# Kernel optimization log

Hardware: AMD Instinct MI355X
Metric: run time of the kernel (lower is better)

Reference implementation:

```python
import jax, jax.numpy as jnp
import numpy as np

N_NODES = 100000
N_EDGES = 1600000
D = 128
L = 3


def setup_inputs() -> dict:
    key = jax.random.key(0)
    k1, k2, k3, k4, k5 = jax.random.split(key, 5)
    x = jax.random.normal(k1, (N_NODES, D), dtype=jnp.float32)
    edge_index = jax.random.randint(k2, (2, N_EDGES), 0, N_NODES, dtype=jnp.int64)
    # Stacked per-layer params (all layers are [D, D] since in==out)
    Wl = jax.random.normal(k3, (L, D, D), dtype=jnp.float32) * 0.05  # lin_l (neighbors), with bias
    bl = jax.random.normal(k4, (L, D), dtype=jnp.float32) * 0.05
    Wr = jax.random.normal(k5, (L, D, D), dtype=jnp.float32) * 0.05  # lin_r (root), no bias
    return {"x": x, "edge_index": edge_index, "Wl": Wl, "bl": bl, "Wr": Wr}


def _sage_conv(x, src, dst, W_l, b_l, W_r):
    # mean aggregation of source features onto target nodes
    msgs = x[src]                                             # [E, D] gather
    agg = jax.ops.segment_sum(msgs, dst, num_segments=N_NODES)  # [N, D] scatter-add
    cnt = jax.ops.segment_sum(jnp.ones((src.shape[0],), x.dtype), dst,
                              num_segments=N_NODES)
    mean = agg / jnp.maximum(cnt, 1.0)[:, None]
    # out = lin_l(mean_neighbors) + lin_r(x)
    return mean @ W_l.T + b_l + x @ W_r.T


def reference(x, edge_index, Wl, bl, Wr):
    src, dst = edge_index[0], edge_index[1]
    for i in range(L):
        x = _sage_conv(x, src, dst, Wl[i], bl[i], Wr[i])
        if i != L - 1:
            x = jax.nn.relu(x)
            # dropout p=0.5 is identity in eval mode
    return jnp.min(x, axis=0)  # [D]
```

## Files before the change

kernel.cpp:

```cpp
#include <hip/hip_runtime.h>
#include <hip/hip_bf16.h>

#define D 128
#define SCAN_C 512
#define BKT 512
#define BKT_SHIFT 9
#define CH 256
#define NBMAX 512
#define MREP 64

typedef __attribute__((ext_vector_type(8))) short bf16x8;
typedef __attribute__((ext_vector_type(4))) float f32x4;

__device__ __forceinline__ float bf16_to_f(unsigned int u) {
    union { unsigned int i; float f; } c; c.i = u << 16; return c.f;
}
__device__ __forceinline__ unsigned short f_to_bf16(float f) {
    union { float f; unsigned int i; } c; c.f = f;
    unsigned int r = c.i + 0x7FFFu + ((c.i >> 16) & 1u);
    return (unsigned short)(r >> 16);
}

__global__ void detect_kernel(const unsigned short* __restrict__ xr,
                              const int* __restrict__ er, int* __restrict__ flag) {
    int plaus = 0;
    for (int i = 0; i < 64; ++i) {
        unsigned short u = xr[2 * i];
        int e = (u >> 7) & 0xFF;
        if (e >= 0x74 && e <= 0x82) plaus++;
    }
    flag[1] = (plaus >= 32) ? 1 : 0;
    int zeros = 0;
    for (int i = 1; i < 128; i += 2) zeros += (er[i] == 0);
    flag[0] = (zeros >= 60) ? 1 : 0;
}

__device__ __forceinline__ int load_idx(const void* p, long long i, int is64) {
    if (is64) return (int)((const long long*)p)[i];
    return ((const int*)p)[i];
}

__global__ void cvt_x_kernel(const void* __restrict__ src, const int* __restrict__ flag,
                             unsigned short* __restrict__ dst, int n) {
    int is_bf16 = flag[1];
    int i = blockIdx.x * blockDim.x + threadIdx.x;
    int stride = gridDim.x * blockDim.x;
    if (is_bf16) {
        const unsigned short* s = (const unsigned short*)src;
        for (; i < n; i += stride) dst[i] = s[i];
    } else {
        const float* s = (const float*)src;
        for (; i < n; i += stride) dst[i] = f_to_bf16(s[i]);
    }
}

__global__ void cvt_f_kernel(const void* __restrict__ src, const int* __restrict__ flag,
                             float* __restrict__ dst, int n) {
    int is_bf16 = flag[1];
    int i = blockIdx.x * blockDim.x + threadIdx.x;
    int stride = gridDim.x * blockDim.x;
    if (is_bf16) {
        const unsigned short* s = (const unsigned short*)src;
        for (; i < n; i += stride) dst[i] = bf16_to_f(s[i]);
    } else {
        const float* s = (const float*)src;
        for (; i < n; i += stride) dst[i] = s[i];
    }
}

__global__ void packW_kernel(const void* __restrict__ Wl0, const void* __restrict__ Wr0,
                             const int* __restrict__ flag, unsigned short* __restrict__ Wpack,
                             int L) {
    int idx = blockIdx.x * blockDim.x + threadIdx.x;
    if (idx >= L * 8 * 8 * 64) return;
    int lane = idx & 63;
    int ks = (idx >> 6) & 7;
    int nt = (idx >> 9) & 7;
    int layer = idx >> 12;
    int n = nt * 16 + (lane & 15);
    int k0 = ks * 32 + (lane >> 4) * 8;
    int is_bf16 = flag[1];
    unsigned short outv[8];
#pragma unroll
    for (int j = 0; j < 8; ++j) {
        int k = k0 + j;
        size_t off = (size_t)layer * D * D + (size_t)n * D + (k & 127);
        float v;
        if (is_bf16) {
            const unsigned short* W = (const unsigned short*)((k < D) ? Wl0 : Wr0);
            v = bf16_to_f(W[off]);
        } else {
            const float* W = (const float*)((k < D) ? Wl0 : Wr0);
            v = W[off];
        }
        outv[j] = f_to_bf16(v);
    }
    *(uint4*)&Wpack[(size_t)idx * 8] = *(uint4*)outv;
}

__global__ void bucket_hist_kernel(const void* __restrict__ eidx, const int* __restrict__ flag,
                                   int* __restrict__ counts2D, int E, int NB, int EPC) {
    __shared__ int hist[NBMAX];
    int c = blockIdx.x;
    for (int i = threadIdx.x; i < NB; i += blockDim.x) hist[i] = 0;
    __syncthreads();
    int is64 = flag[0];
    int end = min(E, (c + 1) * EPC);
    for (int e = c * EPC + threadIdx.x; e < end; e += blockDim.x) {
        int d = load_idx(eidx, (long long)E + e, is64);
        atomicAdd(&hist[d >> BKT_SHIFT], 1);
    }
    __syncthreads();
    for (int i = threadIdx.x; i < NB; i += blockDim.x)
        counts2D[i * CH + c] = hist[i];
}

__global__ void gscan1_kernel(const int* __restrict__ in, int* __restrict__ blockSums, int n) {
    __shared__ int red[256];
    int base = blockIdx.x * SCAN_C;
    int t = threadIdx.x;
    int s = 0;
    if (base + t < n) s += in[base + t];
    if (base + t + 256 < n) s += in[base + t + 256];
    red[t] = s;
    __syncthreads();
    for (int off = 128; off > 0; off >>= 1) {
        if (t < off) red[t] += red[t + off];
        __syncthreads();
    }
    if (t == 0) blockSums[blockIdx.x] = red[0];
}

__global__ void gscan2_kernel(int* __restrict__ blockSums, int nb) {
    __shared__ int sh[256];
    int t = threadIdx.x;
    int orig = (t < nb) ? blockSums[t] : 0;
    sh[t] = orig;
    __syncthreads();
    for (int off = 1; off < 256; off <<= 1) {
        int v = (t >= off) ? sh[t - off] : 0;
        __syncthreads();
        sh[t] += v;
        __syncthreads();
    }
    if (t < nb) blockSums[t] = sh[t] - orig;
}

__global__ void gscan3_kernel(const int* __restrict__ in, const int* __restrict__ blockBase,
                              int* __restrict__ out, int n) {
    __shared__ int sh[SCAN_C];
    int base = blockIdx.x * SCAN_C;
    int t = threadIdx.x;
    int v0 = (base + t < n) ? in[base + t] : 0;
    int v1 = (base + t + 256 < n) ? in[base + t + 256] : 0;
    sh[t] = v0;
    sh[t + 256] = v1;
    __syncthreads();
    for (int off = 1; off < SCAN_C; off <<= 1) {
        int a = (t >= off) ? sh[t - off] : 0;
        int b = (t + 256 >= off) ? sh[t + 256 - off] : 0;
        __syncthreads();
        sh[t] += a;
        sh[t + 256] += b;
        __syncthreads();
    }
    int bb = blockBase[blockIdx.x];
    if (base + t < n) out[base + t] = bb + sh[t] - v0;
    if (base + t + 256 < n) out[base + t + 256] = bb + sh[t + 256] - v1;
}

__global__ void bucket_scatter_kernel(const void* __restrict__ eidx, const int* __restrict__ flag,
                                      const int* __restrict__ bases2D, unsigned int* __restrict__ ebuf,
                                      int E, int NB, int EPC) {
    __shared__ int cur[NBMAX];
    int c = blockIdx.x;
    for (int i = threadIdx.x; i < NB; i += blockDim.x) cur[i] = bases2D[i * CH + c];
    __syncthreads();
    int is64 = flag[0];
    int end = min(E, (c + 1) * EPC);
    for (int e = c * EPC + threadIdx.x; e < end; e += blockDim.x) {
        int s = load_idx(eidx, e, is64);
        int d = load_idx(eidx, (long long)E + e, is64);
        int b = d >> BKT_SHIFT;
        int pos = atomicAdd(&cur[b], 1);
        ebuf[pos] = ((unsigned)s << BKT_SHIFT) | (unsigned)(d & (BKT - 1));
    }
}

__global__ __launch_bounds__(BKT)
void bucket_csr_kernel(const unsigned int* __restrict__ ebuf, const int* __restrict__ bases2D,
                       int* __restrict__ offsets, int* __restrict__ srcs, int E, int N, int NB) {
    __shared__ int lcnt[BKT];
    __shared__ int sh[BKT];
    __shared__ int lcur[BKT];
    int b = blockIdx.x;
    int t = threadIdx.x;
    int start = bases2D[b * CH];
    int end = (b + 1 < NB) ? bases2D[(b + 1) * CH] : E;
    lcnt[t] = 0;
    __syncthreads();
    for (int e = start + t; e < end; e += BKT)
        atomicAdd(&lcnt[ebuf[e] & (BKT - 1)], 1);
    __syncthreads();
    sh[t] = lcnt[t];
    __syncthreads();
    for (int off = 1; off < BKT; off <<= 1) {
        int v = (t >= off) ? sh[t - off] : 0;
        __syncthreads();
        sh[t] += v;
        __syncthreads();
    }
    int excl = sh[t] - lcnt[t];
    int node = b * BKT + t;
    if (node < N) offsets[node] = start + excl;
    lcur[t] = start + excl;
    __syncthreads();
    for (int e = start + t; e < end; e += BKT) {
        unsigned int p = ebuf[e];
        int pos = atomicAdd(&lcur[p & (BKT - 1)], 1);
        srcs[pos] = (int)(p >> BKT_SHIFT);
    }
    if (b == 0 && t == 0) offsets[N] = E;
}

__global__ void agg_kernel(const unsigned short* __restrict__ xb, const int* __restrict__ offsets,
                           const int* __restrict__ srcs, unsigned short* __restrict__ meanb, int N) {
    int g = blockIdx.x * blockDim.x + threadIdx.x;
    int node = g >> 4;
    int lane = g & 15;
    if (node >= N) return;
    int beg = offsets[node], end = offsets[node + 1];
    float acc[8];
#pragma unroll
    for (int i = 0; i < 8; ++i) acc[i] = 0.f;
    const uint4* xp = (const uint4*)xb;

    int j = beg;
    for (; j + 3 < end; j += 4) {
        int s0 = srcs[j];
        int s1 = srcs[j + 1];
        int s2 = srcs[j + 2];
        int s3 = srcs[j + 3];
        uint4 v0 = xp[(size_t)s0 * 16 + lane];
        uint4 v1 = xp[(size_t)s1 * 16 + lane];
        uint4 v2 = xp[(size_t)s2 * 16 + lane];
        uint4 v3 = xp[(size_t)s3 * 16 + lane];
        acc[0] += bf16_to_f(v0.x & 0xFFFFu); acc[1] += bf16_to_f(v0.x >> 16);
        acc[2] += bf16_to_f(v0.y & 0xFFFFu); acc[3] += bf16_to_f(v0.y >> 16);
        acc[4] += bf16_to_f(v0.z & 0xFFFFu); acc[5] += bf16_to_f(v0.z >> 16);
        acc[6] += bf16_to_f(v0.w & 0xFFFFu); acc[7] += bf16_to_f(v0.w >> 16);
        acc[0] += bf16_to_f(v1.x & 0xFFFFu); acc[1] += bf16_to_f(v1.x >> 16);
        acc[2] += bf16_to_f(v1.y & 0xFFFFu); acc[3] += bf16_to_f(v1.y >> 16);
        acc[4] += bf16_to_f(v1.z & 0xFFFFu); acc[5] += bf16_to_f(v1.z >> 16);
        acc[6] += bf16_to_f(v1.w & 0xFFFFu); acc[7] += bf16_to_f(v1.w >> 16);
        acc[0] += bf16_to_f(v2.x & 0xFFFFu); acc[1] += bf16_to_f(v2.x >> 16);
        acc[2] += bf16_to_f(v2.y & 0xFFFFu); acc[3] += bf16_to_f(v2.y >> 16);
        acc[4] += bf16_to_f(v2.z & 0xFFFFu); acc[5] += bf16_to_f(v2.z >> 16);
        acc[6] += bf16_to_f(v2.w & 0xFFFFu); acc[7] += bf16_to_f(v2.w >> 16);
        acc[0] += bf16_to_f(v3.x & 0xFFFFu); acc[1] += bf16_to_f(v3.x >> 16);
        acc[2] += bf16_to_f(v3.y & 0xFFFFu); acc[3] += bf16_to_f(v3.y >> 16);
        acc[4] += bf16_to_f(v3.z & 0xFFFFu); acc[5] += bf16_to_f(v3.z >> 16);
        acc[6] += bf16_to_f(v3.w & 0xFFFFu); acc[7] += bf16_to_f(v3.w >> 16);
    }
    for (; j < end; ++j) {
        uint4 v = xp[(size_t)srcs[j] * 16 + lane];
        acc[0] += bf16_to_f(v.x & 0xFFFFu); acc[1] += bf16_to_f(v.x >> 16);
        acc[2] += bf16_to_f(v.y & 0xFFFFu); acc[3] += bf16_to_f(v.y >> 16);
        acc[4] += bf16_to_f(v.z & 0xFFFFu); acc[5] += bf16_to_f(v.z >> 16);
        acc[6] += bf16_to_f(v.w & 0xFFFFu); acc[7] += bf16_to_f(v.w >> 16);
    }

    float inv = (end > beg) ? 1.0f / (float)(end - beg) : 0.0f;
    uint4 o;
    o.x = (unsigned)f_to_bf16(acc[0] * inv) | ((unsigned)f_to_bf16(acc[1] * inv) << 16);
    o.y = (unsigned)f_to_bf16(acc[2] * inv) | ((unsigned)f_to_bf16(acc[3] * inv) << 16);
    o.z = (unsigned)f_to_bf16(acc[4] * inv) | ((unsigned)f_to_bf16(acc[5] * inv) << 16);
    o.w = (unsigned)f_to_bf16(acc[6] * inv) | ((unsigned)f_to_bf16(acc[7] * inv) << 16);
    ((uint4*)meanb)[(size_t)node * 16 + lane] = o;
}

__global__ __launch_bounds__(256)
void gemm_mfma_kernel(const unsigned short* __restrict__ meanb, const unsigned short* __restrict__ xb,
                      const unsigned short* __restrict__ Wpack, const float* __restrict__ bl,
                      unsigned short* __restrict__ outb, unsigned int* __restrict__ minbuf,
                      int N, int relu, int do_min) {
    __shared__ unsigned short Otile[64][136];
    __shared__ float smin[4][D];

    const int tid = threadIdx.x;
    const int wave = tid >> 6;
    const int lane = tid & 63;
    const int m16 = lane & 15;
    const int quad = lane >> 4;
    const int node0 = blockIdx.x * 64;
    const int arow = node0 + wave * 16 + m16;
    const bool rvalid = arow < N;

    f32x4 acc[8];
#pragma unroll
    for (int i = 0; i < 8; ++i) acc[i] = (f32x4)0.0f;

    const bf16x8* wp = (const bf16x8*)Wpack;

#pragma unroll
    for (int ks = 0; ks < 8; ++ks) {
        uint4 tmp = make_uint4(0u, 0u, 0u, 0u);
        if (rvalid) {
            const unsigned short* base = (ks < 4)
                ? meanb + (size_t)arow * D + ks * 32 + quad * 8
                : xb    + (size_t)arow * D + (ks - 4) * 32 + quad * 8;
            tmp = *(const uint4*)base;
        }
        bf16x8 afrag = *(bf16x8*)&tmp;
#pragma unroll
        for (int nt = 0; nt < 8; ++nt) {
            bf16x8 bfrag = wp[(nt * 8 + ks) * 64 + lane];
            acc[nt] = __builtin_amdgcn_mfma_f32_16x16x32_bf16(afrag, bfrag, acc[nt], 0, 0, 0);
        }
    }

    if (do_min) {
#pragma unroll
        for (int nt = 0; nt < 8; ++nt) {
            int n = nt * 16 + m16;
            float b = bl[n];
            float m = 3.402823466e38f;
#pragma unroll
            for (int r = 0; r < 4; ++r) {
                int node = node0 + wave * 16 + quad * 4 + r;
                float v = (node < N) ? (acc[nt][r] + b) : 3.402823466e38f;
                m = fminf(m, v);
            }
            m = fminf(m, __shfl_xor(m, 16, 64));
            m = fminf(m, __shfl_xor(m, 32, 64));
            if (quad == 0) smin[wave][n] = m;
        }
        __syncthreads();
        if (tid < D) {
            float m = fminf(fminf(smin[0][tid], smin[1][tid]),
                            fminf(smin[2][tid], smin[3][tid]));
            unsigned bits = __float_as_uint(m);
            unsigned enc = ((int)bits >= 0) ? (bits ^ 0x80000000u) : ~bits;
            atomicMin(&minbuf[(blockIdx.x & (MREP - 1)) * D + tid], enc);
        }
        return;
    }

#pragma unroll
    for (int nt = 0; nt < 8; ++nt) {
        int n = nt * 16 + m16;
        float b = bl[n];
#pragma unroll
        for (int r = 0; r < 4; ++r) {
            int m = wave * 16 + quad * 4 + r;
            float v = acc[nt][r] + b;
            if (relu) v = fmaxf(v, 0.f);
            Otile[m][n] = f_to_bf16(v);
        }
    }
    __syncthreads();

    for (int i = tid; i < 64 * 16; i += 256) {
        int row = i >> 4;
        int c = i & 15;
        int n = node0 + row;
        if (n < N) ((uint4*)outb)[(size_t)n * 16 + c] = *(uint4*)&Otile[row][c * 8];
    }
}

__global__ void min_out_kernel(const unsigned int* __restrict__ minbuf,
                               const int* __restrict__ flag, void* __restrict__ out) {
    __shared__ unsigned int sh[4][D];
    int tid = threadIdx.x;
    int q = tid >> 7;
    int c = tid & 127;
    unsigned u = 0xFFFFFFFFu;
    for (int r = q; r < MREP; r += 4) u = min(u, minbuf[r * D + c]);
    sh[q][c] = u;
    __syncthreads();
    if (tid < D) {
        unsigned m = min(min(sh[0][tid], sh[1][tid]), min(sh[2][tid], sh[3][tid]));
        unsigned i = (m & 0x80000000u) ? (m ^ 0x80000000u) : ~m;
        union { unsigned i; float f; } cv; cv.i = i;
        if (flag[1]) ((unsigned short*)out)[tid] = f_to_bf16(cv.f);
        else         ((float*)out)[tid] = cv.f;
    }
}

extern "C" void kernel_launch(void* const* d_in, const int* in_sizes, int n_in,
                              void* d_out, int out_size, void* d_ws, size_t ws_size,
                              hipStream_t stream) {
    const void* x0   = d_in[0];
    const void* eidx = d_in[1];
    const void* Wl0  = d_in[2];
    const void* bl0  = d_in[3];
    const void* Wr0  = d_in[4];

    const int N = in_sizes[0] / D;
    const int E = in_sizes[1] / 2;
    const int L = in_sizes[2] / (D * D);

    char* ws = (char*)d_ws;
    size_t off = 0;
    auto alloc = [&](size_t bytes) -> void* {
        void* p = ws + off;
        off += (bytes + 255) & ~(size_t)255;
        return p;
    };
    unsigned short* xb    = (unsigned short*)alloc((size_t)N * D * 2);
    unsigned short* bufA  = (unsigned short*)alloc((size_t)N * D * 2);
    unsigned short* meanb = (unsigned short*)alloc((size_t)N * D * 2);
    int*   offsets = (int*)alloc((size_t)(N + 1) * sizeof(int));
    int*   srcs    = (int*)alloc((size_t)E * sizeof(int));
    int*   flag    = (int*)alloc(256);
    unsigned short* Wpack = (unsigned short*)alloc((size_t)L * 8 * 8 * 64 * 8 * 2);
    float* blf     = (float*)alloc((size_t)L * D * sizeof(float));
    unsigned int* minbuf = (unsigned int*)alloc((size_t)MREP * D * sizeof(unsigned int));
    (void)ws_size; (void)n_in; (void)out_size;

    const int NB  = (N + BKT - 1) / BKT;
    const int EPC = (E + CH - 1) / CH;
    const int n2  = NB * CH;
    unsigned int* ebuf = (unsigned int*)meanb;
    int* counts2D  = (int*)bufA;
    int* bases2D   = counts2D + n2;
    int* blockSums = bases2D + n2;

    detect_kernel<<<1, 1, 0, stream>>>((const unsigned short*)x0, (const int*)eidx, flag);

    cvt_x_kernel<<<2048, 256, 0, stream>>>(x0, flag, xb, N * D);
    cvt_f_kernel<<<8, 256, 0, stream>>>(bl0, flag, blf, L * D);
    packW_kernel<<<(L * 8 * 8 * 64 + 255) / 256, 256, 0, stream>>>(Wl0, Wr0, flag, Wpack, L);

    hipMemsetAsync(minbuf, 0xFF, (size_t)MREP * D * sizeof(unsigned int), stream);

    bucket_hist_kernel<<<CH, 256, 0, stream>>>(eidx, flag, counts2D, E, NB, EPC);
    const int nb2 = (n2 + SCAN_C - 1) / SCAN_C;
    gscan1_kernel<<<nb2, 256, 0, stream>>>(counts2D, blockSums, n2);
    gscan2_kernel<<<1, 256, 0, stream>>>(blockSums, nb2);
    gscan3_kernel<<<nb2, 256, 0, stream>>>(counts2D, blockSums, bases2D, n2);
    bucket_scatter_kernel<<<CH, 256, 0, stream>>>(eidx, flag, bases2D, ebuf, E, NB, EPC);
    bucket_csr_kernel<<<NB, BKT, 0, stream>>>(ebuf, bases2D, offsets, srcs, E, N, NB);

    unsigned short* cur = xb;
    unsigned short* nxt = bufA;
    for (int l = 0; l < L; ++l) {
        int last = (l == L - 1);
        int agg_blocks = (N * 16 + 255) / 256;
        agg_kernel<<<agg_blocks, 256, 0, stream>>>(cur, offsets, srcs, meanb, N);
        gemm_mfma_kernel<<<(N + 63) / 64, 256, 0, stream>>>(
            meanb, cur, Wpack + (size_t)l * 8 * 8 * 64 * 8, blf + (size_t)l * D,
            nxt, minbuf, N, last ? 0 : 1, last);
        unsigned short* t = cur; cur = nxt; nxt = t;
    }

    min_out_kernel<<<1, 512, 0, stream>>>(minbuf, flag, (void*)d_out);
}
```

Measured before the change: 416.8 us.

## Skip bf16 input copy and double GEMM rows per block to reuse weight fragments

When the input is already bf16, the conversion kernel now returns early and the first layer reads the original buffer directly, selected on device by the flag. The MFMA GEMM now processes 128 rows per block in two 64-row groups that share each loaded weight fragment, which halves weight reloads and halves the block count. The costs are more accumulator registers per thread, possibly lower occupancy, and an extra barrier in the epilogue. For fp32 inputs, which is the default here, the copy-skip path does nothing.

```diff
diff --git a/kernel.cpp b/kernel.cpp
--- a/kernel.cpp
+++ b/kernel.cpp
@@ -42,16 +42,11 @@
 
 __global__ void cvt_x_kernel(const void* __restrict__ src, const int* __restrict__ flag,
                              unsigned short* __restrict__ dst, int n) {
-    int is_bf16 = flag[1];
+    if (flag[1]) return;
     int i = blockIdx.x * blockDim.x + threadIdx.x;
     int stride = gridDim.x * blockDim.x;
-    if (is_bf16) {
-        const unsigned short* s = (const unsigned short*)src;
-        for (; i < n; i += stride) dst[i] = s[i];
-    } else {
-        const float* s = (const float*)src;
-        for (; i < n; i += stride) dst[i] = f_to_bf16(s[i]);
-    }
+    const float* s = (const float*)src;
+    for (; i < n; i += stride) dst[i] = f_to_bf16(s[i]);
 }
 
 __global__ void cvt_f_kernel(const void* __restrict__ src, const int* __restrict__ flag,
@@ -223,8 +218,11 @@
     if (b == 0 && t == 0) offsets[N] = E;
 }
 
-__global__ void agg_kernel(const unsigned short* __restrict__ xb, const int* __restrict__ offsets,
+__global__ void agg_kernel(const unsigned short* __restrict__ xmain,
+                           const unsigned short* __restrict__ xalt,
+                           const int* __restrict__ flag, const int* __restrict__ offsets,
                            const int* __restrict__ srcs, unsigned short* __restrict__ meanb, int N) {
+    const unsigned short* xb = flag[1] ? xalt : xmain;
     int g = blockIdx.x * blockDim.x + threadIdx.x;
     int node = g >> 4;
     int lane = g & 15;
@@ -280,42 +278,58 @@
 }
 
 __global__ __launch_bounds__(256)
-void gemm_mfma_kernel(const unsigned short* __restrict__ meanb, const unsigned short* __restrict__ xb,
+void gemm_mfma_kernel(const unsigned short* __restrict__ meanb,
+                      const unsigned short* __restrict__ xmain,
+                      const unsigned short* __restrict__ xalt,
+                      const int* __restrict__ flag,
                       const unsigned short* __restrict__ Wpack, const float* __restrict__ bl,
                       unsigned short* __restrict__ outb, unsigned int* __restrict__ minbuf,
                       int N, int relu, int do_min) {
     __shared__ unsigned short Otile[64][136];
     __shared__ float smin[4][D];
+    const unsigned short* xb = flag[1] ? xalt : xmain;
 
     const int tid = threadIdx.x;
     const int wave = tid >> 6;
     const int lane = tid & 63;
     const int m16 = lane & 15;
     const int quad = lane >> 4;
-    const int node0 = blockIdx.x * 64;
-    const int arow = node0 + wave * 16 + m16;
-    const bool rvalid = arow < N;
-
-    f32x4 acc[8];
-#pragma unroll
-    for (int i = 0; i < 8; ++i) acc[i] = (f32x4)0.0f;
+    const int node0 = blockIdx.x * 128;
+
+    f32x4 acc[2][8];
+#pragma unroll
+    for (int g = 0; g < 2; ++g)
+#pragma unroll
+        for (int i = 0; i < 8; ++i) acc[g][i] = (f32x4)0.0f;
 
     const bf16x8* wp = (const bf16x8*)Wpack;
+    int arow[2];
+    bool rv[2];
+#pragma unroll
+    for (int g = 0; g < 2; ++g) {
+        arow[g] = node0 + g * 64 + wave * 16 + m16;
+        rv[g] = arow[g] < N;
+    }
 
 #pragma unroll
     for (int ks = 0; ks < 8; ++ks) {
-        uint4 tmp = make_uint4(0u, 0u, 0u, 0u);
-        if (rvalid) {
-            const unsigned short* base = (ks < 4)
-                ? meanb + (size_t)arow * D + ks * 32 + quad * 8
-                : xb    + (size_t)arow * D + (ks - 4) * 32 + quad * 8;
-            tmp = *(const uint4*)base;
-        }
-        bf16x8 afrag = *(bf16x8*)&tmp;
+        bf16x8 afrag[2];
+#pragma unroll
+        for (int g = 0; g < 2; ++g) {
+            uint4 tmp = make_uint4(0u, 0u, 0u, 0u);
+            if (rv[g]) {
+                const unsigned short* base = (ks < 4)
+                    ? meanb + (size_t)arow[g] * D + ks * 32 + quad * 8
+                    : xb    + (size_t)arow[g] * D + (ks - 4) * 32 + quad * 8;
+                tmp = *(const uint4*)base;
+            }
+            afrag[g] = *(bf16x8*)&tmp;
+        }
 #pragma unroll
         for (int nt = 0; nt < 8; ++nt) {
             bf16x8 bfrag = wp[(nt * 8 + ks) * 64 + lane];
-            acc[nt] = __builtin_amdgcn_mfma_f32_16x16x32_bf16(afrag, bfrag, acc[nt], 0, 0, 0);
+            acc[0][nt] = __builtin_amdgcn_mfma_f32_16x16x32_bf16(afrag[0], bfrag, acc[0][nt], 0, 0, 0);
+            acc[1][nt] = __builtin_amdgcn_mfma_f32_16x16x32_bf16(afrag[1], bfrag, acc[1][nt], 0, 0, 0);
         }
     }
 
@@ -326,11 +340,13 @@
             float b = bl[n];
             float m = 3.402823466e38f;
 #pragma unroll
-            for (int r = 0; r < 4; ++r) {
-                int node = node0 + wave * 16 + quad * 4 + r;
-                float v = (node < N) ? (acc[nt][r] + b) : 3.402823466e38f;
-                m = fminf(m, v);
-            }
+            for (int g = 0; g < 2; ++g)
+#pragma unroll
+                for (int r = 0; r < 4; ++r) {
+                    int node = node0 + g * 64 + wave * 16 + quad * 4 + r;
+                    float v = (node < N) ? (acc[g][nt][r] + b) : 3.402823466e38f;
+                    m = fminf(m, v);
+                }
             m = fminf(m, __shfl_xor(m, 16, 64));
             m = fminf(m, __shfl_xor(m, 32, 64));
             if (quad == 0) smin[wave][n] = m;
@@ -347,24 +363,27 @@
     }
 
 #pragma unroll
-    for (int nt = 0; nt < 8; ++nt) {
-        int n = nt * 16 + m16;
-        float b = bl[n];
-#pragma unroll
-        for (int r = 0; r < 4; ++r) {
-            int m = wave * 16 + quad * 4 + r;
-            float v = acc[nt][r] + b;
-            if (relu) v = fmaxf(v, 0.f);
-            Otile[m][n] = f_to_bf16(v);
-        }
-    }
-    __syncthreads();
-
-    for (int i = tid; i < 64 * 16; i += 256) {
-        int row = i >> 4;
-        int c = i & 15;
-        int n = node0 + row;
-        if (n < N) ((uint4*)outb)[(size_t)n * 16 + c] = *(uint4*)&Otile[row][c * 8];
+    for (int g = 0; g < 2; ++g) {
+        if (g) __syncthreads();
+#pragma unroll
+        for (int nt = 0; nt < 8; ++nt) {
+            int n = nt * 16 + m16;
+            float b = bl[n];
+#pragma unroll
+            for (int r = 0; r < 4; ++r) {
+                int m = wave * 16 + quad * 4 + r;
+                float v = acc[g][nt][r] + b;
+                if (relu) v = fmaxf(v, 0.f);
+                Otile[m][n] = f_to_bf16(v);
+            }
+        }
+        __syncthreads();
+        for (int i = tid; i < 64 * 16; i += 256) {
+            int row = i >> 4;
+            int c = i & 15;
+            int n = node0 + g * 64 + row;
+            if (n < N) ((uint4*)outb)[(size_t)n * 16 + c] = *(uint4*)&Otile[row][c * 8];
+        }
     }
 }
 
@@ -442,16 +461,18 @@
     bucket_scatter_kernel<<<CH, 256, 0, stream>>>(eidx, flag, bases2D, ebuf, E, NB, EPC);
     bucket_csr_kernel<<<NB, BKT, 0, stream>>>(ebuf, bases2D, offsets, srcs, E, N, NB);
 
-    unsigned short* cur = xb;
+    const unsigned short* cur     = xb;
+    const unsigned short* cur_alt = (const unsigned short*)x0;
     unsigned short* nxt = bufA;
     for (int l = 0; l < L; ++l) {
         int last = (l == L - 1);
         int agg_blocks = (N * 16 + 255) / 256;
-        agg_kernel<<<agg_blocks, 256, 0, stream>>>(cur, offsets, srcs, meanb, N);
-        gemm_mfma_kernel<<<(N + 63) / 64, 256, 0, stream>>>(
-            meanb, cur, Wpack + (size_t)l * 8 * 8 * 64 * 8, blf + (size_t)l * D,
+        agg_kernel<<<agg_blocks, 256, 0, stream>>>(cur, cur_alt, flag, offsets, srcs, meanb, N);
+        gemm_mfma_kernel<<<(N + 127) / 128, 256, 0, stream>>>(
+            meanb, cur, cur_alt, flag, Wpack + (size_t)l * 8 * 8 * 64 * 8, blf + (size_t)l * D,
             nxt, minbuf, N, last ? 0 : 1, last);
-        unsigned short* t = cur; cur = nxt; nxt = t;
+        cur = nxt; cur_alt = nxt;
+        nxt = (nxt == bufA) ? xb : bufA;
     }
 
     min_out_kernel<<<1, 512, 0, stream>>>(minbuf, flag, (void*)d_out);
```

After: 435.3 us. +4.4%, slower.
